# Kernel optimization log

Measured on AMD Instinct MI355X. Metric: run time of the kernel, lower is better.

The kernel has to match this reference:

```python
import jax, jax.numpy as jnp
import numpy as np

T, B, D, H, F, E = 2048, 2, 1024, 16, 4096, 8
HD = D // H
EPS = 1.1920929e-07  # torch.finfo(float32).eps


def setup_inputs() -> dict:
    key = jax.random.key(0)
    ks = jax.random.split(key, 20)
    sc = D ** -0.5
    n = lambda k, shape, s: jax.random.normal(k, shape, jnp.float32) * s
    return {
        "x": jax.random.normal(ks[0], (T, B, D), jnp.float32),
        "Wq": n(ks[1], (D, D), sc), "bq": jnp.zeros((D,), jnp.float32),
        "Wk": n(ks[2], (D, D), sc), "bk": jnp.zeros((D,), jnp.float32),
        "Wv": n(ks[3], (D, D), sc), "bv": jnp.zeros((D,), jnp.float32),
        "Wo": n(ks[4], (D, D), sc), "bo": jnp.zeros((D,), jnp.float32),
        "ln1_g": jnp.ones((D,), jnp.float32), "ln1_b": jnp.zeros((D,), jnp.float32),
        "ln2_g": jnp.ones((D,), jnp.float32), "ln2_b": jnp.zeros((D,), jnp.float32),
        "wg": n(ks[5], (D, E), sc),
        "W1": n(ks[6], (E, D, F), sc), "b1": jnp.zeros((E, F), jnp.float32),
        "W2": n(ks[7], (E, F, D), F ** -0.5), "b2": jnp.zeros((E, D), jnp.float32),
    }


def layer_norm(x, g, b):
    m = jnp.mean(x, -1, keepdims=True)
    v = jnp.var(x, -1, keepdims=True)
    return (x - m) * jax.lax.rsqrt(v + 1e-5) * g + b


def attention(x, Wq, bq, Wk, bk, Wv, bv, Wo, bo):
    t, b, d = x.shape
    q = ((x @ Wq + bq) * (HD ** -0.5)).reshape(t, b, H, HD)
    k = (x @ Wk + bk).reshape(t, b, H, HD)
    v = (x @ Wv + bv).reshape(t, b, H, HD)
    a = jax.nn.softmax(jnp.einsum('tbhd,sbhd->bhts', q, k), axis=-1)
    o = jnp.einsum('bhts,sbhd->tbhd', a, v).reshape(t, b, d)
    return o @ Wo + bo


def moe(xf, wg, W1, b1, W2, b2):
    # xf: [S, D] tokens (batch-major order, matching x.transpose(0,1).reshape(-1,d))
    S = xf.shape[0]
    C = 2 * ((S + E - 1) // E)  # fairseq top2 train capacity
    logits = xf.astype(jnp.float32) @ wg.astype(jnp.float32)
    gates = jax.nn.softmax(logits, axis=-1)
    idx1 = jnp.argmax(gates, axis=-1)
    m1 = jax.nn.one_hot(idx1, E, dtype=jnp.int32)
    idx2 = jnp.argmax(jnp.where(m1 > 0, -jnp.inf, logits), axis=-1)
    m2 = jax.nn.one_hot(idx2, E, dtype=jnp.int32)
    g1 = jnp.take_along_axis(gates, idx1[:, None], 1)[:, 0]
    g2 = jnp.take_along_axis(gates, idx2[:, None], 1)[:, 0]
    loc1 = jnp.cumsum(m1, axis=0) - 1
    loc2 = jnp.cumsum(m2, axis=0) - 1 + jnp.sum(m1, axis=0, keepdims=True)
    pos1 = jnp.sum(loc1 * m1, axis=1)
    pos2 = jnp.sum(loc2 * m2, axis=1)
    l_aux = jnp.mean(jnp.mean(gates, 0) * jnp.mean(m1.astype(jnp.float32), 0)) * E * E
    k1 = (pos1 < C).astype(xf.dtype)
    k2 = (pos2 < C).astype(xf.dtype)
    g1 = g1.astype(xf.dtype) * k1
    g2 = g2.astype(xf.dtype) * k2
    den = jnp.maximum(g1 + g2, EPS)
    g1, g2 = g1 / den, g2 / den
    f1 = idx1 * C + jnp.minimum(pos1, C - 1)
    f2 = idx2 * C + jnp.minimum(pos2, C - 1)
    # dispatch (unweighted, capacity-masked)
    buf = jnp.zeros((E * C, D), xf.dtype)
    buf = buf.at[f1].add(xf * k1[:, None]).at[f2].add(xf * k2[:, None])
    h = jax.nn.relu(jnp.einsum('ecd,edf->ecf', buf.reshape(E, C, D), W1) + b1[:, None, :])
    out = (jnp.einsum('ecf,efd->ecd', h, W2) + b2[:, None, :]).reshape(E * C, D)
    # combine with normalized gates (dropped tokens have zero gate)
    y = g1[:, None] * out[f1] + g2[:, None] * out[f2]
    return y, l_aux


def reference(x, Wq, bq, Wk, bk, Wv, bv, Wo, bo, ln1_g, ln1_b, ln2_g, ln2_b, wg, W1, b1, W2, b2):
    # pre-LN self-attention block
    residual = x
    h = layer_norm(x, ln1_g, ln1_b)
    h = attention(h, Wq, bq, Wk, bk, Wv, bv, Wo, bo)
    x = residual + h
    # pre-LN MoE FFN block
    residual = x
    h = layer_norm(x, ln2_g, ln2_b)
    hb = jnp.swapaxes(h, 0, 1).reshape(-1, D)  # [B*T, D]
    y, l_aux = moe(hb, wg, W1, b1, W2, b2)
    y = jnp.swapaxes(y.reshape(B, T, D), 0, 1)
    x = residual + y
    return x, l_aux
```

## Files before the change

### kernel.cpp

```cpp
#include <hip/hip_runtime.h>

#define TT 2048
#define BB 2
#define DD 1024
#define HH 16
#define HD 64
#define FF 4096
#define EE 8
#define SS (TT*BB)
#define CAP 1024
#define EPSF 1.1920929e-07f

typedef __attribute__((ext_vector_type(8))) short short8;
typedef __attribute__((ext_vector_type(4))) float floatx4;

static __device__ inline unsigned short f2bf(float f){
    unsigned int u = __float_as_uint(f);
    unsigned int r = (u + 0x7fffu + ((u>>16)&1u)) >> 16;
    return (unsigned short)r;
}
static __device__ inline float bf2f(unsigned short h){
    return __uint_as_float(((unsigned int)h)<<16);
}
static __device__ inline void split2(float x, unsigned short& h, unsigned short& l){
    unsigned short hh = f2bf(x);
    h = hh;
    l = f2bf(x - bf2f(hh));
}
#define GETF4(v,j) ((j)==0?(v).x:(j)==1?(v).y:(j)==2?(v).z:(v).w)
#define GETU4(v,j) ((j)==0?(v).x:(j)==1?(v).y:(j)==2?(v).z:(v).w)

__global__ __launch_bounds__(256) void ln_kernel(const float* __restrict__ x,
    const float* __restrict__ gam, const float* __restrict__ bet, float* __restrict__ o)
{
    int row = blockIdx.x;
    int tid = threadIdx.x;
    float4 v = ((const float4*)(x + (size_t)row*DD))[tid];
    float s  = v.x+v.y+v.z+v.w;
    float ss = v.x*v.x+v.y*v.y+v.z*v.z+v.w*v.w;
    __shared__ float r1[256], r2[256];
    r1[tid]=s; r2[tid]=ss;
    __syncthreads();
    for (int off=128; off>0; off>>=1){
        if (tid<off){ r1[tid]+=r1[tid+off]; r2[tid]+=r2[tid+off]; }
        __syncthreads();
    }
    float mean = r1[0] * (1.f/DD);
    float var  = r2[0] * (1.f/DD) - mean*mean;
    float inv  = 1.f / sqrtf(var + 1e-5f);
    float4 g = ((const float4*)gam)[tid];
    float4 b = ((const float4*)bet)[tid];
    float4 r;
    r.x = (v.x-mean)*inv*g.x + b.x;
    r.y = (v.y-mean)*inv*g.y + b.y;
    r.z = (v.z-mean)*inv*g.z + b.z;
    r.w = (v.w-mean)*inv*g.w + b.w;
    ((float4*)(o + (size_t)row*DD))[tid] = r;
}

__global__ __launch_bounds__(256) void ln_split_kernel(const float* __restrict__ x,
    const float* __restrict__ gam, const float* __restrict__ bet,
    unsigned short* __restrict__ oh, unsigned short* __restrict__ ol)
{
    int row = blockIdx.x;
    int tid = threadIdx.x;
    float4 v = ((const float4*)(x + (size_t)row*DD))[tid];
    float s  = v.x+v.y+v.z+v.w;
    float ss = v.x*v.x+v.y*v.y+v.z*v.z+v.w*v.w;
    __shared__ float r1[256], r2[256];
    r1[tid]=s; r2[tid]=ss;
    __syncthreads();
    for (int off=128; off>0; off>>=1){
        if (tid<off){ r1[tid]+=r1[tid+off]; r2[tid]+=r2[tid+off]; }
        __syncthreads();
    }
    float mean = r1[0] * (1.f/DD);
    float var  = r2[0] * (1.f/DD) - mean*mean;
    float inv  = 1.f / sqrtf(var + 1e-5f);
    float4 g = ((const float4*)gam)[tid];
    float4 b = ((const float4*)bet)[tid];
    float4 r;
    r.x = (v.x-mean)*inv*g.x + b.x;
    r.y = (v.y-mean)*inv*g.y + b.y;
    r.z = (v.z-mean)*inv*g.z + b.z;
    r.w = (v.w-mean)*inv*g.w + b.w;
    ushort4 hv, lv;
    split2(r.x, hv.x, lv.x);
    split2(r.y, hv.y, lv.y);
    split2(r.z, hv.z, lv.z);
    split2(r.w, hv.w, lv.w);
    ((ushort4*)(oh + (size_t)row*DD))[tid] = hv;
    ((ushort4*)(ol + (size_t)row*DD))[tid] = lv;
}

template<bool RELU, bool OUTBF16>
__global__ __launch_bounds__(256) void gemm_mfma(
    const unsigned short* __restrict__ A, const unsigned short* __restrict__ Bt,
    const float* __restrict__ bias, float* __restrict__ Cf,
    unsigned short* __restrict__ Cb,
    int M, int N, int K, long wStride, int bStride, int rowsPerExp)
{
    __shared__ unsigned short As[128*64];
    __shared__ unsigned short Bs[128*64];
    const int tid = threadIdx.x, lane = tid&63;
    const int w = tid>>6, wr = w>>1, wc = w&1;
    const int m0 = blockIdx.y*128, n0 = blockIdx.x*128;
    const int e = m0 / rowsPerExp;
    const unsigned short* Bp = Bt + (size_t)e*wStride;
    const int srow = tid>>3, sslot = tid&7;
    floatx4 zf = {0.f,0.f,0.f,0.f};
    floatx4 acc[4][4];
    #pragma unroll
    for (int m=0;m<4;m++)
        #pragma unroll
        for (int n=0;n<4;n++) acc[m][n]=zf;

    short8 ar[4], br[4];
    #pragma unroll
    for (int i=0;i<4;i++){
        int r = srow + i*32;
        ar[i] = *(const short8*)(A  + (size_t)(m0+r)*K + sslot*8);
        br[i] = *(const short8*)(Bp + (size_t)(n0+r)*K + sslot*8);
    }
    const int NT = K/64;
    for (int kt=0; kt<NT; kt++){
        __syncthreads();
        #pragma unroll
        for (int i=0;i<4;i++){
            int r = srow + i*32;
            int off = r*64 + ((sslot ^ (r&7))<<3);
            *(short8*)(&As[off]) = ar[i];
            *(short8*)(&Bs[off]) = br[i];
        }
        __syncthreads();
        if (kt+1 < NT){
            int k0 = (kt+1)*64;
            #pragma unroll
            for (int i=0;i<4;i++){
                int r = srow + i*32;
                ar[i] = *(const short8*)(A  + (size_t)(m0+r)*K + k0 + sslot*8);
                br[i] = *(const short8*)(Bp + (size_t)(n0+r)*K + k0 + sslot*8);
            }
        }
        #pragma unroll
        for (int kk=0;kk<2;kk++){
            short8 af[4], bf[4];
            int kgrp = kk*4 + (lane>>4);
            #pragma unroll
            for (int m=0;m<4;m++){
                int rowa = wr*64 + m*16 + (lane&15);
                af[m] = *(const short8*)(&As[rowa*64 + ((kgrp ^ (rowa&7))<<3)]);
                int rowb = wc*64 + m*16 + (lane&15);
                bf[m] = *(const short8*)(&Bs[rowb*64 + ((kgrp ^ (rowb&7))<<3)]);
            }
            #pragma unroll
            for (int m=0;m<4;m++)
                #pragma unroll
                for (int n=0;n<4;n++)
                    acc[m][n] = __builtin_amdgcn_mfma_f32_16x16x32_bf16(af[m], bf[n], acc[m][n], 0,0,0);
        }
    }
    int colg = n0 + wc*64 + (lane&15);
    int rowg = m0 + wr*64 + ((lane>>4)<<2);
    #pragma unroll
    for (int n=0;n<4;n++){
        float bv = bias[e*bStride + colg + n*16];
        #pragma unroll
        for (int m=0;m<4;m++){
            #pragma unroll
            for (int i2=0;i2<4;i2++){
                float v = acc[m][n][i2] + bv;
                if (RELU) v = fmaxf(v, 0.f);
                size_t o = (size_t)(rowg + m*16 + i2)*N + colg + n*16;
                if (OUTBF16) Cb[o] = f2bf(v); else Cf[o] = v;
            }
        }
    }
}

template<bool QKV>
__global__ __launch_bounds__(256) void gemm_mfma_s(
    const unsigned short* __restrict__ Ahi, const unsigned short* __restrict__ Alo,
    const unsigned short* __restrict__ Bhi, const unsigned short* __restrict__ Blo,
    const float* __restrict__ b0, const float* __restrict__ b1p, const float* __restrict__ b2p,
    const float* __restrict__ res,
    float* __restrict__ o0,
    unsigned short* __restrict__ kh, unsigned short* __restrict__ kl,
    unsigned short* __restrict__ vh, unsigned short* __restrict__ vl,
    int M, int K)
{
    __shared__ unsigned short As[128*64];
    __shared__ unsigned short Bs[128*64];
    const int tid = threadIdx.x, lane = tid&63;
    const int w = tid>>6, wr = w>>1, wc = w&1;
    const int m0 = blockIdx.y*128, n0 = blockIdx.x*128;
    const int row = tid>>1, khalf = tid&1;
    floatx4 zf = {0.f,0.f,0.f,0.f};
    floatx4 acc[4][4];
    #pragma unroll
    for (int m=0;m<4;m++)
        #pragma unroll
        for (int n=0;n<4;n++) acc[m][n]=zf;

    short8 awh0,awh1,awl0,awl1, bwh0,bwh1,bwl0,bwl1;
    {
        size_t ao = (size_t)(m0+row)*K + khalf*16;
        awh0 = *(const short8*)(Ahi+ao); awh1 = *(const short8*)(Ahi+ao+8);
        awl0 = *(const short8*)(Alo+ao); awl1 = *(const short8*)(Alo+ao+8);
        size_t bo = (size_t)(n0+row)*K + khalf*16;
        bwh0 = *(const short8*)(Bhi+bo); bwh1 = *(const short8*)(Bhi+bo+8);
        bwl0 = *(const short8*)(Blo+bo); bwl1 = *(const short8*)(Blo+bo+8);
    }
    const int NT = K/32;
    for (int kt=0; kt<NT; kt++){
        __syncthreads();
        {
            int base = row*64, sw = row&7;
            int g0 = khalf*2, g1 = khalf*2+1;
            *(short8*)(&As[base + ((g0^sw)<<3)])     = awh0;
            *(short8*)(&As[base + ((g1^sw)<<3)])     = awh1;
            *(short8*)(&As[base + (((g0+4)^sw)<<3)]) = awl0;
            *(short8*)(&As[base + (((g1+4)^sw)<<3)]) = awl1;
            *(short8*)(&Bs[base + ((g0^sw)<<3)])     = bwh0;
            *(short8*)(&Bs[base + ((g1^sw)<<3)])     = bwh1;
            *(short8*)(&Bs[base + (((g0+4)^sw)<<3)]) = bwl0;
            *(short8*)(&Bs[base + (((g1+4)^sw)<<3)]) = bwl1;
        }
        __syncthreads();
        if (kt+1 < NT){
            int k0 = (kt+1)*32;
            size_t ao = (size_t)(m0+row)*K + k0 + khalf*16;
            awh0 = *(const short8*)(Ahi+ao); awh1 = *(const short8*)(Ahi+ao+8);
            awl0 = *(const short8*)(Alo+ao); awl1 = *(const short8*)(Alo+ao+8);
            size_t bo = (size_t)(n0+row)*K + k0 + khalf*16;
            bwh0 = *(const short8*)(Bhi+bo); bwh1 = *(const short8*)(Bhi+bo+8);
            bwl0 = *(const short8*)(Blo+bo); bwl1 = *(const short8*)(Blo+bo+8);
        }
        {
            int kg = lane>>4;
            short8 afh[4], afl[4], bfh[4], bfl[4];
            #pragma unroll
            for (int m=0;m<4;m++){
                int ra = wr*64 + m*16 + (lane&15);
                afh[m] = *(const short8*)(&As[ra*64 + ((kg ^ (ra&7))<<3)]);
                afl[m] = *(const short8*)(&As[ra*64 + (((kg+4) ^ (ra&7))<<3)]);
                int rb = wc*64 + m*16 + (lane&15);
                bfh[m] = *(const short8*)(&Bs[rb*64 + ((kg ^ (rb&7))<<3)]);
                bfl[m] = *(const short8*)(&Bs[rb*64 + (((kg+4) ^ (rb&7))<<3)]);
            }
            #pragma unroll
            for (int m=0;m<4;m++)
                #pragma unroll
                for (int n=0;n<4;n++){
                    acc[m][n] = __builtin_amdgcn_mfma_f32_16x16x32_bf16(afl[m], bfh[n], acc[m][n], 0,0,0);
                    acc[m][n] = __builtin_amdgcn_mfma_f32_16x16x32_bf16(afh[m], bfl[n], acc[m][n], 0,0,0);
                    acc[m][n] = __builtin_amdgcn_mfma_f32_16x16x32_bf16(afh[m], bfh[n], acc[m][n], 0,0,0);
                }
        }
    }
    int colg = n0 + wc*64 + (lane&15);
    int rowg = m0 + wr*64 + ((lane>>4)<<2);
    if (QKV){
        int chunk = n0>>10;
        int colc = colg & 1023;
        const float* bp = chunk==0 ? b0 : (chunk==1 ? b1p : b2p);
        #pragma unroll
        for (int n=0;n<4;n++){
            float bv = bp[colc + n*16];
            #pragma unroll
            for (int m=0;m<4;m++){
                #pragma unroll
                for (int i2=0;i2<4;i2++){
                    int r = rowg + m*16 + i2;
                    float v = acc[m][n][i2] + bv;
                    size_t off = (size_t)r*DD + colc + n*16;
                    if (chunk==0){
                        o0[off] = v*0.125f;
                    } else {
                        unsigned short hh, ll;
                        split2(v, hh, ll);
                        if (chunk==1){ kh[off]=hh; kl[off]=ll; }
                        else         { vh[off]=hh; vl[off]=ll; }
                    }
                }
            }
        }
    } else {
        #pragma unroll
        for (int n=0;n<4;n++){
            float bv = b0[colg + n*16];
            #pragma unroll
            for (int m=0;m<4;m++){
                #pragma unroll
                for (int i2=0;i2<4;i2++){
                    int r = rowg + m*16 + i2;
                    float v = acc[m][n][i2] + bv + res[(size_t)r*DD + colg + n*16];
                    o0[(size_t)r*DD + colg + n*16] = v;
                }
            }
        }
    }
}

__global__ __launch_bounds__(512) void attn_mfma(const float* __restrict__ q,
    const unsigned short* __restrict__ khi, const unsigned short* __restrict__ klo,
    const unsigned short* __restrict__ vhi, const unsigned short* __restrict__ vlo,
    unsigned short* __restrict__ ohi, unsigned short* __restrict__ olo)
{
    __shared__ unsigned short Kh[64*64], Kl[64*64];
    __shared__ unsigned short Vh[64*64], Vl[64*64];
    __shared__ unsigned short Ph[8*16*64];
    const int tid = threadIdx.x, lane = tid&63, w = tid>>6;
    const int t0 = blockIdx.x*128;
    const int b = blockIdx.y>>4, h = blockIdx.y&15;

    short8 qh[2], ql[2];
    #pragma unroll
    for (int kk=0;kk<2;kk++){
        const float* qp = q + ((size_t)(t0 + 16*w + (lane&15))*BB + b)*DD + h*64 + kk*32 + (lane>>4)*8;
        float4 f0 = ((const float4*)qp)[0];
        float4 f1 = ((const float4*)qp)[1];
        unsigned short hh[8], ll[8];
        #pragma unroll
        for (int j=0;j<4;j++){ split2(GETF4(f0,j), hh[j], ll[j]); }
        #pragma unroll
        for (int j=0;j<4;j++){ split2(GETF4(f1,j), hh[4+j], ll[4+j]); }
        qh[kk] = *(short8*)hh; ql[kk] = *(short8*)ll;
    }

    const int kr = tid>>3, kq = tid&7;
    const int vs0 = (tid&31)*2, vd0 = (tid>>5)*4;
    short8 kwh, kwl;
    ushort4 vwh[2], vwl[2];
    {
        size_t ko = ((size_t)kr*BB + b)*DD + h*64 + kq*8;
        kwh = *(const short8*)(khi + ko);
        kwl = *(const short8*)(klo + ko);
        #pragma unroll
        for (int i=0;i<2;i++){
            size_t vo = ((size_t)(vs0+i)*BB + b)*DD + h*64 + vd0;
            vwh[i] = *(const ushort4*)(vhi + vo);
            vwl[i] = *(const ushort4*)(vlo + vo);
        }
    }

    float m_st[4] = {-3.0e38f,-3.0e38f,-3.0e38f,-3.0e38f};
    float l_st[4] = {0.f,0.f,0.f,0.f};
    floatx4 zf = {0.f,0.f,0.f,0.f};
    floatx4 oacc[4];
    #pragma unroll
    for (int n=0;n<4;n++) oacc[n]=zf;

    for (int s0=0; s0<TT; s0+=64){
        __syncthreads();
        {
            int off = kr*64 + ((kq ^ (kr&7))<<3);
            *(short8*)(&Kh[off]) = kwh;
            *(short8*)(&Kl[off]) = kwl;
        }
        {
            int g = vs0>>3, so = vs0&7;
            #pragma unroll
            for (int j=0;j<4;j++){
                int d = vd0 + j;
                ushort2 hv, lv;
                hv.x=GETU4(vwh[0],j); hv.y=GETU4(vwh[1],j);
                lv.x=GETU4(vwl[0],j); lv.y=GETU4(vwl[1],j);
                int off = d*64 + ((g ^ (d&7))<<3) + so;
                *(ushort2*)(&Vh[off]) = hv;
                *(ushort2*)(&Vl[off]) = lv;
            }
        }
        __syncthreads();
        if (s0+64 < TT){
            size_t ko = ((size_t)(s0+64+kr)*BB + b)*DD + h*64 + kq*8;
            kwh = *(const short8*)(khi + ko);
            kwl = *(const short8*)(klo + ko);
            #pragma unroll
            for (int i=0;i<2;i++){
                size_t vo = ((size_t)(s0+64+vs0+i)*BB + b)*DD + h*64 + vd0;
                vwh[i] = *(const ushort4*)(vhi + vo);
                vwl[i] = *(const ushort4*)(vlo + vo);
            }
        }
        floatx4 sacc[4];
        __builtin_amdgcn_s_setprio(1);
        #pragma unroll
        for (int n=0;n<4;n++){
            floatx4 s = zf;
            #pragma unroll
            for (int kk=0;kk<2;kk++){
                int g = kk*4 + (lane>>4);
                int rb = n*16 + (lane&15);
                short8 kbh = *(const short8*)(&Kh[rb*64 + ((g ^ (rb&7))<<3)]);
                short8 kbl = *(const short8*)(&Kl[rb*64 + ((g ^ (rb&7))<<3)]);
                s = __builtin_amdgcn_mfma_f32_16x16x32_bf16(ql[kk], kbh, s, 0,0,0);
                s = __builtin_amdgcn_mfma_f32_16x16x32_bf16(qh[kk], kbl, s, 0,0,0);
                s = __builtin_amdgcn_mfma_f32_16x16x32_bf16(qh[kk], kbh, s, 0,0,0);
            }
            sacc[n] = s;
        }
        __builtin_amdgcn_s_setprio(0);
        float mx[4];
        #pragma unroll
        for (int r=0;r<4;r++)
            mx[r] = fmaxf(fmaxf(sacc[0][r], sacc[1][r]), fmaxf(sacc[2][r], sacc[3][r]));
        #pragma unroll
        for (int sh=1; sh<16; sh<<=1){
            #pragma unroll
            for (int r=0;r<4;r++) mx[r] = fmaxf(mx[r], __shfl_xor(mx[r], sh));
        }
        float corr[4];
        #pragma unroll
        for (int r=0;r<4;r++){
            float nm = fmaxf(m_st[r], mx[r]);
            corr[r] = __expf(m_st[r] - nm);
            m_st[r] = nm;
        }
        float ts[4] = {0.f,0.f,0.f,0.f};
        #pragma unroll
        for (int n=0;n<4;n++){
            #pragma unroll
            for (int r=0;r<4;r++){
                float p = __expf(sacc[n][r] - m_st[r]);
                ts[r] += p;
                int q2 = ((lane>>4)<<2) + r;
                int s2 = n*16 + (lane&15);
                int off = w*1024 + q2*64 + (((s2>>3) ^ (q2&7))<<3) + (s2&7);
                Ph[off] = f2bf(p);
            }
        }
        #pragma unroll
        for (int sh=1; sh<16; sh<<=1){
            #pragma unroll
            for (int r=0;r<4;r++) ts[r] += __shfl_xor(ts[r], sh);
        }
        #pragma unroll
        for (int r=0;r<4;r++) l_st[r] = l_st[r]*corr[r] + ts[r];
        #pragma unroll
        for (int n=0;n<4;n++)
            #pragma unroll
            for (int r=0;r<4;r++) oacc[n][r] *= corr[r];
        __builtin_amdgcn_s_setprio(1);
        #pragma unroll
        for (int kk=0;kk<2;kk++){
            int g = kk*4 + (lane>>4);
            int rq = lane&15;
            short8 pa = *(const short8*)(&Ph[w*1024 + rq*64 + ((g ^ (rq&7))<<3)]);
            #pragma unroll
            for (int n=0;n<4;n++){
                int rd = n*16 + (lane&15);
                short8 vbh = *(const short8*)(&Vh[rd*64 + ((g ^ (rd&7))<<3)]);
                short8 vbl = *(const short8*)(&Vl[rd*64 + ((g ^ (rd&7))<<3)]);
                oacc[n] = __builtin_amdgcn_mfma_f32_16x16x32_bf16(pa, vbl, oacc[n], 0,0,0);
                oacc[n] = __builtin_amdgcn_mfma_f32_16x16x32_bf16(pa, vbh, oacc[n], 0,0,0);
            }
        }
        __builtin_amdgcn_s_setprio(0);
    }
    float il[4];
    #pragma unroll
    for (int r=0;r<4;r++) il[r] = 1.f/l_st[r];
    int qrow = t0 + 16*w + ((lane>>4)<<2);
    #pragma unroll
    for (int n=0;n<4;n++){
        #pragma unroll
        for (int r=0;r<4;r++){
            float v = oacc[n][r]*il[r];
            unsigned short hh, ll;
            split2(v, hh, ll);
            size_t off = ((size_t)(qrow+r)*BB + b)*DD + h*64 + n*16 + (lane&15);
            ohi[off] = hh; olo[off] = ll;
        }
    }
}

__global__ __launch_bounds__(256) void transpose_bf16_k(const float* __restrict__ in,
    unsigned short* __restrict__ outp, int R, int C)
{
    __shared__ float t[64][65];
    int e = blockIdx.z;
    const float* ip = in + (size_t)e*R*C;
    unsigned short* op = outp + (size_t)e*R*C;
    int r0 = blockIdx.y*64, c0 = blockIdx.x*64;
    int tid = threadIdx.x;
    #pragma unroll
    for (int i=0;i<4;i++){
        int ch = i*256 + tid;
        int r = ch>>4, c4 = (ch&15)*4;
        float4 v = *(const float4*)(ip + (size_t)(r0+r)*C + c0 + c4);
        t[r][c4+0]=v.x; t[r][c4+1]=v.y; t[r][c4+2]=v.z; t[r][c4+3]=v.w;
    }
    __syncthreads();
    #pragma unroll
    for (int i=0;i<4;i++){
        int ch = i*256 + tid;
        int rr = ch>>4, c4 = (ch&15)*4;
        ushort4 o;
        o.x = f2bf(t[c4+0][rr]); o.y = f2bf(t[c4+1][rr]);
        o.z = f2bf(t[c4+2][rr]); o.w = f2bf(t[c4+3][rr]);
        *(ushort4*)(op + (size_t)(c0+rr)*R + r0 + c4) = o;
    }
}

__global__ __launch_bounds__(256) void transpose_split_k(const float* __restrict__ in,
    unsigned short* __restrict__ oh, unsigned short* __restrict__ ol, int R, int C)
{
    __shared__ float t[64][65];
    int r0 = blockIdx.y*64, c0 = blockIdx.x*64;
    int tid = threadIdx.x;
    #pragma unroll
    for (int i=0;i<4;i++){
        int ch = i*256 + tid;
        int r = ch>>4, c4 = (ch&15)*4;
        float4 v = *(const float4*)(in + (size_t)(r0+r)*C + c0 + c4);
        t[r][c4+0]=v.x; t[r][c4+1]=v.y; t[r][c4+2]=v.z; t[r][c4+3]=v.w;
    }
    __syncthreads();
    #pragma unroll
    for (int i=0;i<4;i++){
        int ch = i*256 + tid;
        int rr = ch>>4, c4 = (ch&15)*4;
        ushort4 hv, lv;
        split2(t[c4+0][rr], hv.x, lv.x);
        split2(t[c4+1][rr], hv.y, lv.y);
        split2(t[c4+2][rr], hv.z, lv.z);
        split2(t[c4+3][rr], hv.w, lv.w);
        size_t off = (size_t)(c0+rr)*R + r0 + c4;
        *(ushort4*)(oh + off) = hv;
        *(ushort4*)(ol + off) = lv;
    }
}

__global__ __launch_bounds__(256) void gather_bf16_k(const float* __restrict__ h2,
    const int* __restrict__ s2r, unsigned short* __restrict__ buf)
{
    int s = blockIdx.x; int row = s2r[s]; int c = threadIdx.x;
    float4 v = make_float4(0.f,0.f,0.f,0.f);
    if (row>=0) v = *(const float4*)(h2 + (size_t)row*DD + c*4);
    ushort4 o;
    o.x=f2bf(v.x); o.y=f2bf(v.y); o.z=f2bf(v.z); o.w=f2bf(v.w);
    *(ushort4*)(buf + (size_t)s*DD + c*4) = o;
}

__global__ __launch_bounds__(256) void route_kernel(const float* __restrict__ h2,
    const float* __restrict__ wgm, float* __restrict__ gates,
    int* __restrict__ idx1, int* __restrict__ idx2,
    float* __restrict__ g1, float* __restrict__ g2)
{
    int wid = threadIdx.x >> 6, lane = threadIdx.x & 63;
    int s = blockIdx.x*4 + wid;
    int row = (s % TT)*BB + (s / TT);
    const float* hr = h2 + (size_t)row*DD;
    float acc[EE] = {};
    #pragma unroll
    for (int c=0;c<16;c++){
        int d = c*64 + lane;
        float xv = hr[d];
        const float* wr = wgm + (size_t)d*EE;
        #pragma unroll
        for (int e2=0;e2<EE;e2++) acc[e2] += xv * wr[e2];
    }
    #pragma unroll
    for (int off=32; off>0; off>>=1){
        #pragma unroll
        for (int e2=0;e2<EE;e2++) acc[e2] += __shfl_down(acc[e2], off);
    }
    if (lane==0){
        float mx = acc[0];
        #pragma unroll
        for (int e2=1;e2<EE;e2++) mx = fmaxf(mx, acc[e2]);
        float ex[EE]; float sum=0.f;
        #pragma unroll
        for (int e2=0;e2<EE;e2++){ ex[e2] = __expf(acc[e2]-mx); sum += ex[e2]; }
        float inv = 1.f/sum;
        int i1=0; float bv1=acc[0];
        #pragma unroll
        for (int e2=1;e2<EE;e2++){ if (acc[e2] > bv1){ bv1=acc[e2]; i1=e2; } }
        int i2=-1; float bv2=-3.0e38f;
        #pragma unroll
        for (int e2=0;e2<EE;e2++){ if (e2!=i1 && acc[e2] > bv2){ bv2=acc[e2]; i2=e2; } }
        #pragma unroll
        for (int e2=0;e2<EE;e2++) gates[(size_t)s*EE + e2] = ex[e2]*inv;
        idx1[s]=i1; idx2[s]=i2;
        g1[s]=ex[i1]*inv; g2[s]=ex[i2]*inv;
    }
}

__global__ __launch_bounds__(256) void scan_kernel(
    const float* __restrict__ gates, const int* __restrict__ idx1, const int* __restrict__ idx2,
    const float* __restrict__ g1, const float* __restrict__ g2,
    float* __restrict__ g1n, float* __restrict__ g2n,
    int* __restrict__ f1, int* __restrict__ f2, int* __restrict__ slot2row,
    float* __restrict__ laux)
{
    __shared__ int i1s[SS];
    __shared__ int i2s[SS];
    __shared__ int cnt1[256][EE];
    __shared__ int cnt2[256][EE];
    __shared__ float gsum[256][EE];
    __shared__ int tot1[EE];
    int tid = threadIdx.x;
    for (int i=tid;i<EE*CAP;i+=256) slot2row[i] = -1;
    for (int i=tid;i<SS;i+=256){ i1s[i]=idx1[i]; i2s[i]=idx2[i]; }
    __syncthreads();
    int c1l[EE]={}, c2l[EE]={};
    float gl[EE]={};
    int base = tid*16;
    for (int qq=0;qq<16;qq++){
        int s = base+qq;
        c1l[i1s[s]]++; c2l[i2s[s]]++;
        #pragma unroll
        for (int e2=0;e2<EE;e2++) gl[e2] += gates[(size_t)s*EE+e2];
    }
    #pragma unroll
    for (int e2=0;e2<EE;e2++){ cnt1[tid][e2]=c1l[e2]; cnt2[tid][e2]=c2l[e2]; gsum[tid][e2]=gl[e2]; }
    __syncthreads();
    if (tid < EE){
        int e2 = tid;
        int run=0;
        for (int t=0;t<256;t++){ int tmp=cnt1[t][e2]; cnt1[t][e2]=run; run+=tmp; }
        tot1[e2]=run;
        run=0;
        for (int t=0;t<256;t++){ int tmp=cnt2[t][e2]; cnt2[t][e2]=run; run+=tmp; }
        float gr=0.f;
        for (int t=0;t<256;t++) gr += gsum[t][e2];
        gsum[0][e2]=gr;
    }
    __syncthreads();
    int p1[EE], p2[EE];
    #pragma unroll
    for (int e2=0;e2<EE;e2++){ p1[e2]=cnt1[tid][e2]; p2[e2]=cnt2[tid][e2]+tot1[e2]; }
    for (int qq=0;qq<16;qq++){
        int s = base+qq;
        int e1 = i1s[s], e2v = i2s[s];
        int pos1 = p1[e1]++;
        int pos2 = p2[e2v]++;
        float gv1 = g1[s], gv2 = g2[s];
        float gm1 = (pos1<CAP)? gv1 : 0.f;
        float gm2 = (pos2<CAP)? gv2 : 0.f;
        float den = fmaxf(gm1+gm2, EPSF);
        g1n[s] = gm1/den; g2n[s] = gm2/den;
        int ff1 = e1*CAP + (pos1<CAP?pos1:CAP-1);
        int ff2 = e2v*CAP + (pos2<CAP?pos2:CAP-1);
        f1[s]=ff1; f2[s]=ff2;
        int hrow = (s % TT)*BB + (s / TT);
        if (pos1<CAP) slot2row[ff1]=hrow;
        if (pos2<CAP) slot2row[ff2]=hrow;
    }
    if (tid==0){
        float a=0.f;
        #pragma unroll
        for (int e2=0;e2<EE;e2++) a += (gsum[0][e2]*(1.f/SS)) * ((float)tot1[e2]*(1.f/SS));
        laux[0] = a * (float)EE;
    }
}

__global__ __launch_bounds__(256) void combine_kernel(const float* __restrict__ x2,
    const float* __restrict__ eout, const float* __restrict__ g1n, const float* __restrict__ g2n,
    const int* __restrict__ f1, const int* __restrict__ f2, float* __restrict__ out)
{
    int s = blockIdx.x;
    float a = g1n[s], b = g2n[s];
    int s1 = f1[s], s2 = f2[s];
    int row = (s % TT)*BB + (s / TT);
    int c = threadIdx.x;
    float4 o1 = ((const float4*)(eout + (size_t)s1*DD))[c];
    float4 o2 = ((const float4*)(eout + (size_t)s2*DD))[c];
    float4 xr = ((const float4*)(x2 + (size_t)row*DD))[c];
    float4 r;
    r.x = xr.x + a*o1.x + b*o2.x;
    r.y = xr.y + a*o1.y + b*o2.y;
    r.z = xr.z + a*o1.z + b*o2.z;
    r.w = xr.w + a*o1.w + b*o2.w;
    ((float4*)(out + (size_t)row*DD))[c] = r;
}

extern "C" void kernel_launch(void* const* d_in, const int* in_sizes, int n_in,
                              void* d_out, int out_size, void* d_ws, size_t ws_size,
                              hipStream_t stream)
{
    const float* x    = (const float*)d_in[0];
    const float* Wq   = (const float*)d_in[1];
    const float* bq   = (const float*)d_in[2];
    const float* Wk   = (const float*)d_in[3];
    const float* bk   = (const float*)d_in[4];
    const float* Wv   = (const float*)d_in[5];
    const float* bv   = (const float*)d_in[6];
    const float* Wo   = (const float*)d_in[7];
    const float* bo   = (const float*)d_in[8];
    const float* ln1g = (const float*)d_in[9];
    const float* ln1b = (const float*)d_in[10];
    const float* ln2g = (const float*)d_in[11];
    const float* ln2b = (const float*)d_in[12];
    const float* wgm  = (const float*)d_in[13];
    const float* W1   = (const float*)d_in[14];
    const float* b1   = (const float*)d_in[15];
    const float* W2   = (const float*)d_in[16];
    const float* b2   = (const float*)d_in[17];
    float* out = (float*)d_out;

    char* w = (char*)d_ws;
    unsigned short* h1hi = (unsigned short*)(w);
    unsigned short* h1lo = (unsigned short*)(w + ((size_t)8<<20));
    float*          qb   = (float*)(w + ((size_t)16<<20));
    unsigned short* Khg  = (unsigned short*)(w + ((size_t)32<<20));
    unsigned short* Klg  = (unsigned short*)(w + ((size_t)40<<20));
    unsigned short* Vhg  = (unsigned short*)(w + ((size_t)48<<20));
    unsigned short* Vlg  = (unsigned short*)(w + ((size_t)56<<20));
    float*          x2   = (float*)(w + ((size_t)64<<20));
    unsigned short* bufb = (unsigned short*)(w + ((size_t)80<<20));
    unsigned short* hb   = (unsigned short*)(w + ((size_t)96<<20));
    unsigned short* Bqkv_hi = (unsigned short*)(w + ((size_t)96<<20));
    unsigned short* Bqkv_lo = (unsigned short*)(w + ((size_t)102<<20));
    unsigned short* Bo_hi   = (unsigned short*)(w + ((size_t)108<<20));
    unsigned short* Bo_lo   = (unsigned short*)(w + ((size_t)110<<20));
    unsigned short* W1t  = (unsigned short*)(w + ((size_t)160<<20));
    unsigned short* W2t  = (unsigned short*)(w + ((size_t)224<<20));
    float*          ffno = (float*)(w + ((size_t)32<<20));
    char*  sm   = w + ((size_t)288<<20);
    float* gates   = (float*)(sm);                sm += (size_t)SS*EE*4;
    int*   idx1    = (int*)(sm);                  sm += SS*4;
    int*   idx2    = (int*)(sm);                  sm += SS*4;
    float* g1      = (float*)(sm);                sm += SS*4;
    float* g2      = (float*)(sm);                sm += SS*4;
    float* g1n     = (float*)(sm);                sm += SS*4;
    float* g2n     = (float*)(sm);                sm += SS*4;
    int*   f1      = (int*)(sm);                  sm += SS*4;
    int*   f2      = (int*)(sm);                  sm += SS*4;
    int*   slot2row= (int*)(sm);                  sm += EE*CAP*4;

    transpose_bf16_k<<<dim3(FF/64, DD/64, EE), 256, 0, stream>>>(W1, W1t, DD, FF);
    transpose_bf16_k<<<dim3(DD/64, FF/64, EE), 256, 0, stream>>>(W2, W2t, FF, DD);
    transpose_split_k<<<dim3(16,16), 256, 0, stream>>>(Wq, Bqkv_hi,                   Bqkv_lo,                   DD, DD);
    transpose_split_k<<<dim3(16,16), 256, 0, stream>>>(Wk, Bqkv_hi + (size_t)DD*DD,   Bqkv_lo + (size_t)DD*DD,   DD, DD);
    transpose_split_k<<<dim3(16,16), 256, 0, stream>>>(Wv, Bqkv_hi + (size_t)2*DD*DD, Bqkv_lo + (size_t)2*DD*DD, DD, DD);
    transpose_split_k<<<dim3(16,16), 256, 0, stream>>>(Wo, Bo_hi, Bo_lo, DD, DD);
    ln_split_kernel<<<SS, 256, 0, stream>>>(x, ln1g, ln1b, h1hi, h1lo);
    gemm_mfma_s<true><<<dim3(24, SS/128), 256, 0, stream>>>(
        h1hi, h1lo, Bqkv_hi, Bqkv_lo, bq, bk, bv, nullptr, qb, Khg, Klg, Vhg, Vlg, SS, DD);
    attn_mfma<<<dim3(TT/128, BB*HH), 512, 0, stream>>>(qb, Khg, Klg, Vhg, Vlg, h1hi, h1lo);
    gemm_mfma_s<false><<<dim3(8, SS/128), 256, 0, stream>>>(
        h1hi, h1lo, Bo_hi, Bo_lo, bo, bo, bo, x, x2, nullptr, nullptr, nullptr, nullptr, SS, DD);
    ln_kernel<<<SS, 256, 0, stream>>>(x2, ln2g, ln2b, qb);
    route_kernel<<<SS/4, 256, 0, stream>>>(qb, wgm, gates, idx1, idx2, g1, g2);
    scan_kernel<<<1, 256, 0, stream>>>(gates, idx1, idx2, g1, g2,
        g1n, g2n, f1, f2, slot2row, out + (size_t)SS*DD);
    gather_bf16_k<<<EE*CAP, 256, 0, stream>>>(qb, slot2row, bufb);
    gemm_mfma<true,true><<<dim3(FF/128, (EE*CAP)/128), 256, 0, stream>>>(
        bufb, W1t, b1, nullptr, hb, EE*CAP, FF, DD, (long)FF*DD, FF, CAP);
    gemm_mfma<false,false><<<dim3(DD/128, (EE*CAP)/128), 256, 0, stream>>>(
        hb, W2t, b2, ffno, nullptr, EE*CAP, DD, FF, (long)DD*FF, DD, CAP);
    combine_kernel<<<SS, 256, 0, stream>>>(x2, ffno, g1n, g2n, f1, f2, out);
    (void)in_sizes; (void)n_in; (void)out_size; (void)ws_size;
}
```

Baseline: 666.5 us.

## Store V as single bf16 and double attention key tile to 128

```diff
diff --git a/kernel.cpp b/kernel.cpp
--- a/kernel.cpp
+++ b/kernel.cpp
@@ -28,7 +28,6 @@
     l = f2bf(x - bf2f(hh));
 }
 #define GETF4(v,j) ((j)==0?(v).x:(j)==1?(v).y:(j)==2?(v).z:(v).w)
-#define GETU4(v,j) ((j)==0?(v).x:(j)==1?(v).y:(j)==2?(v).z:(v).w)
 
 __global__ __launch_bounds__(256) void ln_kernel(const float* __restrict__ x,
     const float* __restrict__ gam, const float* __restrict__ bet, float* __restrict__ o)
@@ -186,7 +185,7 @@
     const float* __restrict__ res,
     float* __restrict__ o0,
     unsigned short* __restrict__ kh, unsigned short* __restrict__ kl,
-    unsigned short* __restrict__ vh, unsigned short* __restrict__ vl,
+    unsigned short* __restrict__ vh,
     int M, int K)
 {
     __shared__ unsigned short As[128*64];
@@ -276,11 +275,12 @@
                     size_t off = (size_t)r*DD + colc + n*16;
                     if (chunk==0){
                         o0[off] = v*0.125f;
-                    } else {
+                    } else if (chunk==1){
                         unsigned short hh, ll;
                         split2(v, hh, ll);
-                        if (chunk==1){ kh[off]=hh; kl[off]=ll; }
-                        else         { vh[off]=hh; vl[off]=ll; }
+                        kh[off]=hh; kl[off]=ll;
+                    } else {
+                        vh[off] = f2bf(v);
                     }
                 }
             }
@@ -304,11 +304,11 @@
 
 __global__ __launch_bounds__(512) void attn_mfma(const float* __restrict__ q,
     const unsigned short* __restrict__ khi, const unsigned short* __restrict__ klo,
-    const unsigned short* __restrict__ vhi, const unsigned short* __restrict__ vlo,
+    const unsigned short* __restrict__ vbf,
     unsigned short* __restrict__ ohi, unsigned short* __restrict__ olo)
 {
-    __shared__ unsigned short Kh[64*64], Kl[64*64];
-    __shared__ unsigned short Vh[64*64], Vl[64*64];
+    __shared__ unsigned short Kh[128*64], Kl[128*64];
+    __shared__ unsigned short Vb[64*128];
     __shared__ unsigned short Ph[8*16*64];
     const int tid = threadIdx.x, lane = tid&63, w = tid>>6;
     const int t0 = blockIdx.x*128;
@@ -328,20 +328,16 @@
         qh[kk] = *(short8*)hh; ql[kk] = *(short8*)ll;
     }
 
-    const int kr = tid>>3, kq = tid&7;
-    const int vs0 = (tid&31)*2, vd0 = (tid>>5)*4;
-    short8 kwh, kwl;
-    ushort4 vwh[2], vwl[2];
+    const int kr = tid>>2, kq = tid&3;
+    const int vs0 = (tid&63)*2, vd0 = (tid>>6)*8;
+    short8 kwh0,kwh1,kwl0,kwl1, vw0,vw1;
     {
-        size_t ko = ((size_t)kr*BB + b)*DD + h*64 + kq*8;
-        kwh = *(const short8*)(khi + ko);
-        kwl = *(const short8*)(klo + ko);
-        #pragma unroll
-        for (int i=0;i<2;i++){
-            size_t vo = ((size_t)(vs0+i)*BB + b)*DD + h*64 + vd0;
-            vwh[i] = *(const ushort4*)(vhi + vo);
-            vwl[i] = *(const ushort4*)(vlo + vo);
-        }
+        size_t ko = ((size_t)kr*BB + b)*DD + h*64 + kq*16;
+        kwh0 = *(const short8*)(khi+ko); kwh1 = *(const short8*)(khi+ko+8);
+        kwl0 = *(const short8*)(klo+ko); kwl1 = *(const short8*)(klo+ko+8);
+        size_t vo = ((size_t)vs0*BB + b)*DD + h*64 + vd0;
+        vw0 = *(const short8*)(vbf+vo);
+        vw1 = *(const short8*)(vbf+vo + (size_t)BB*DD);
     }
 
     float m_st[4] = {-3.0e38f,-3.0e38f,-3.0e38f,-3.0e38f};
@@ -351,42 +347,40 @@
     #pragma unroll
     for (int n=0;n<4;n++) oacc[n]=zf;
 
-    for (int s0=0; s0<TT; s0+=64){
+    for (int s0=0; s0<TT; s0+=128){
         __syncthreads();
         {
-            int off = kr*64 + ((kq ^ (kr&7))<<3);
-            *(short8*)(&Kh[off]) = kwh;
-            *(short8*)(&Kl[off]) = kwl;
+            int base = kr*64, sw = kr&7;
+            int g0 = kq*2, g1 = kq*2+1;
+            *(short8*)(&Kh[base + ((g0^sw)<<3)]) = kwh0;
+            *(short8*)(&Kh[base + ((g1^sw)<<3)]) = kwh1;
+            *(short8*)(&Kl[base + ((g0^sw)<<3)]) = kwl0;
+            *(short8*)(&Kl[base + ((g1^sw)<<3)]) = kwl1;
         }
         {
             int g = vs0>>3, so = vs0&7;
             #pragma unroll
-            for (int j=0;j<4;j++){
+            for (int j=0;j<8;j++){
                 int d = vd0 + j;
-                ushort2 hv, lv;
-                hv.x=GETU4(vwh[0],j); hv.y=GETU4(vwh[1],j);
-                lv.x=GETU4(vwl[0],j); lv.y=GETU4(vwl[1],j);
-                int off = d*64 + ((g ^ (d&7))<<3) + so;
-                *(ushort2*)(&Vh[off]) = hv;
-                *(ushort2*)(&Vl[off]) = lv;
+                ushort2 pv;
+                pv.x = (unsigned short)vw0[j];
+                pv.y = (unsigned short)vw1[j];
+                *(ushort2*)(&Vb[d*128 + ((g ^ (d&7))<<3) + so]) = pv;
             }
         }
         __syncthreads();
-        if (s0+64 < TT){
-            size_t ko = ((size_t)(s0+64+kr)*BB + b)*DD + h*64 + kq*8;
-            kwh = *(const short8*)(khi + ko);
-            kwl = *(const short8*)(klo + ko);
-            #pragma unroll
-            for (int i=0;i<2;i++){
-                size_t vo = ((size_t)(s0+64+vs0+i)*BB + b)*DD + h*64 + vd0;
-                vwh[i] = *(const ushort4*)(vhi + vo);
-                vwl[i] = *(const ushort4*)(vlo + vo);
-            }
-        }
-        floatx4 sacc[4];
+        if (s0+128 < TT){
+            size_t ko = ((size_t)(s0+128+kr)*BB + b)*DD + h*64 + kq*16;
+            kwh0 = *(const short8*)(khi+ko); kwh1 = *(const short8*)(khi+ko+8);
+            kwl0 = *(const short8*)(klo+ko); kwl1 = *(const short8*)(klo+ko+8);
+            size_t vo = ((size_t)(s0+128+vs0)*BB + b)*DD + h*64 + vd0;
+            vw0 = *(const short8*)(vbf+vo);
+            vw1 = *(const short8*)(vbf+vo + (size_t)BB*DD);
+        }
+        floatx4 sacc[8];
         __builtin_amdgcn_s_setprio(1);
         #pragma unroll
-        for (int n=0;n<4;n++){
+        for (int n=0;n<8;n++){
             floatx4 s = zf;
             #pragma unroll
             for (int kk=0;kk<2;kk++){
@@ -403,8 +397,11 @@
         __builtin_amdgcn_s_setprio(0);
         float mx[4];
         #pragma unroll
-        for (int r=0;r<4;r++)
-            mx[r] = fmaxf(fmaxf(sacc[0][r], sacc[1][r]), fmaxf(sacc[2][r], sacc[3][r]));
+        for (int r=0;r<4;r++){
+            float a0 = fmaxf(fmaxf(sacc[0][r], sacc[1][r]), fmaxf(sacc[2][r], sacc[3][r]));
+            float a1 = fmaxf(fmaxf(sacc[4][r], sacc[5][r]), fmaxf(sacc[6][r], sacc[7][r]));
+            mx[r] = fmaxf(a0, a1);
+        }
         #pragma unroll
         for (int sh=1; sh<16; sh<<=1){
             #pragma unroll
@@ -419,15 +416,12 @@
         }
         float ts[4] = {0.f,0.f,0.f,0.f};
         #pragma unroll
-        for (int n=0;n<4;n++){
+        for (int n=0;n<8;n++){
             #pragma unroll
             for (int r=0;r<4;r++){
                 float p = __expf(sacc[n][r] - m_st[r]);
                 ts[r] += p;
-                int q2 = ((lane>>4)<<2) + r;
-                int s2 = n*16 + (lane&15);
-                int off = w*1024 + q2*64 + (((s2>>3) ^ (q2&7))<<3) + (s2&7);
-                Ph[off] = f2bf(p);
+                sacc[n][r] = p;
             }
         }
         #pragma unroll
@@ -441,22 +435,35 @@
         for (int n=0;n<4;n++)
             #pragma unroll
             for (int r=0;r<4;r++) oacc[n][r] *= corr[r];
-        __builtin_amdgcn_s_setprio(1);
-        #pragma unroll
-        for (int kk=0;kk<2;kk++){
-            int g = kk*4 + (lane>>4);
-            int rq = lane&15;
-            short8 pa = *(const short8*)(&Ph[w*1024 + rq*64 + ((g ^ (rq&7))<<3)]);
-            #pragma unroll
-            for (int n=0;n<4;n++){
-                int rd = n*16 + (lane&15);
-                short8 vbh = *(const short8*)(&Vh[rd*64 + ((g ^ (rd&7))<<3)]);
-                short8 vbl = *(const short8*)(&Vl[rd*64 + ((g ^ (rd&7))<<3)]);
-                oacc[n] = __builtin_amdgcn_mfma_f32_16x16x32_bf16(pa, vbl, oacc[n], 0,0,0);
-                oacc[n] = __builtin_amdgcn_mfma_f32_16x16x32_bf16(pa, vbh, oacc[n], 0,0,0);
-            }
-        }
-        __builtin_amdgcn_s_setprio(0);
+        #pragma unroll
+        for (int half=0; half<2; half++){
+            #pragma unroll
+            for (int n2=0;n2<4;n2++){
+                int n = half*4 + n2;
+                #pragma unroll
+                for (int r=0;r<4;r++){
+                    int q2 = ((lane>>4)<<2) + r;
+                    int s2 = n2*16 + (lane&15);
+                    int off = w*1024 + q2*64 + (((s2>>3) ^ (q2&7))<<3) + (s2&7);
+                    Ph[off] = f2bf(sacc[n][r]);
+                }
+            }
+            __builtin_amdgcn_s_setprio(1);
+            #pragma unroll
+            for (int kk=0;kk<2;kk++){
+                int g = kk*4 + (lane>>4);
+                int rq = lane&15;
+                short8 pa = *(const short8*)(&Ph[w*1024 + rq*64 + ((g ^ (rq&7))<<3)]);
+                #pragma unroll
+                for (int n=0;n<4;n++){
+                    int rd = n*16 + (lane&15);
+                    int gv = half*8 + g;
+                    short8 vb = *(const short8*)(&Vb[rd*128 + ((gv ^ (rd&7))<<3)]);
+                    oacc[n] = __builtin_amdgcn_mfma_f32_16x16x32_bf16(pa, vb, oacc[n], 0,0,0);
+                }
+            }
+            __builtin_amdgcn_s_setprio(0);
+        }
     }
     float il[4];
     #pragma unroll
@@ -707,7 +714,6 @@
     unsigned short* Khg  = (unsigned short*)(w + ((size_t)32<<20));
     unsigned short* Klg  = (unsigned short*)(w + ((size_t)40<<20));
     unsigned short* Vhg  = (unsigned short*)(w + ((size_t)48<<20));
-    unsigned short* Vlg  = (unsigned short*)(w + ((size_t)56<<20));
     float*          x2   = (float*)(w + ((size_t)64<<20));
     unsigned short* bufb = (unsigned short*)(w + ((size_t)80<<20));
     unsigned short* hb   = (unsigned short*)(w + ((size_t)96<<20));
@@ -738,10 +744,10 @@
     transpose_split_k<<<dim3(16,16), 256, 0, stream>>>(Wo, Bo_hi, Bo_lo, DD, DD);
     ln_split_kernel<<<SS, 256, 0, stream>>>(x, ln1g, ln1b, h1hi, h1lo);
     gemm_mfma_s<true><<<dim3(24, SS/128), 256, 0, stream>>>(
-        h1hi, h1lo, Bqkv_hi, Bqkv_lo, bq, bk, bv, nullptr, qb, Khg, Klg, Vhg, Vlg, SS, DD);
-    attn_mfma<<<dim3(TT/128, BB*HH), 512, 0, stream>>>(qb, Khg, Klg, Vhg, Vlg, h1hi, h1lo);
+        h1hi, h1lo, Bqkv_hi, Bqkv_lo, bq, bk, bv, nullptr, qb, Khg, Klg, Vhg, SS, DD);
+    attn_mfma<<<dim3(TT/128, BB*HH), 512, 0, stream>>>(qb, Khg, Klg, Vhg, h1hi, h1lo);
     gemm_mfma_s<false><<<dim3(8, SS/128), 256, 0, stream>>>(
-        h1hi, h1lo, Bo_hi, Bo_lo, bo, bo, bo, x, x2, nullptr, nullptr, nullptr, nullptr, SS, DD);
+        h1hi, h1lo, Bo_hi, Bo_lo, bo, bo, bo, x, x2, nullptr, nullptr, nullptr, SS, DD);
     ln_kernel<<<SS, 256, 0, stream>>>(x2, ln2g, ln2b, qb);
     route_kernel<<<SS/4, 256, 0, stream>>>(qb, wgm, gates, idx1, idx2, g1, g2);
     scan_kernel<<<1, 256, 0, stream>>>(gates, idx1, idx2, g1, g2,
```

Result: faster. 615.8 us (-7.6%).
